# Performance work log

Hardware: AMD Instinct MI355X
Metric: run time of the kernel (lower is better)

The kernel has to match this reference:

```python
import jax, jax.numpy as jnp
import numpy as np

DIM = 256
HEADS = 8
HD = DIM // HEADS          # 32
WS = 8                     # window size
TOPK = 4
SCALE = HD ** -0.5


def setup_inputs() -> dict:
    key = jax.random.key(0)
    k1, k2, k3 = jax.random.split(key, 3)
    B, H, W = 8, 64, 64
    x = jax.random.normal(k1, (B, DIM, H, W), dtype=jnp.float32)
    # 1x1 conv weights (BN folded -> weight + bias), fan-in scaled to keep logits sane
    w_qkv = jax.random.normal(k2, (3 * DIM, DIM), dtype=jnp.float32) / np.sqrt(DIM)
    b_qkv = jnp.zeros((3 * DIM,), dtype=jnp.float32)
    w_proj = jax.random.normal(k3, (DIM, DIM), dtype=jnp.float32) / np.sqrt(DIM)
    b_proj = jnp.zeros((DIM,), dtype=jnp.float32)
    return {"x": x, "w_qkv": w_qkv, "b_qkv": b_qkv, "w_proj": w_proj, "b_proj": b_proj}


def _window_partition(t, ws):
    # t: [BH, D, H, W] -> [BH, R, ws*ws, D]
    bh, d, h, w = t.shape
    gh, gw = h // ws, w // ws
    t = t.reshape(bh, d, gh, ws, gw, ws)
    t = t.transpose(0, 2, 4, 3, 5, 1)          # [BH, gh, gw, ws, ws, D]
    return t.reshape(bh, gh * gw, ws * ws, d)


def reference(x, w_qkv, b_qkv, w_proj, b_proj):
    B, C, H, W = x.shape
    gh, gw = H // WS, W // WS
    R, T = gh * gw, WS * WS
    BH = B * HEADS

    # qkv 1x1 conv
    qkv = jnp.einsum('bchw,oc->bohw', x, w_qkv) + b_qkv[None, :, None, None]
    q, k, v = jnp.split(qkv, 3, axis=1)                       # each [B, C, H, W]

    def to_bh(t):
        return t.reshape(BH, HD, H, W)

    q_w = _window_partition(to_bh(q), WS)                     # [BH, R, T, HD]
    k_w = _window_partition(to_bh(k), WS)
    v_w = _window_partition(to_bh(v), WS)

    # region-level routing: mean-pooled region tokens
    q_r = q_w.mean(axis=2)                                    # [BH, R, HD]
    k_r = k_w.mean(axis=2)
    attn_r = jnp.einsum('brd,bkd->brk', q_r, k_r) * SCALE     # [BH, R, R]
    topk = min(TOPK, R)
    _, topk_idx = jax.lax.top_k(attn_r, topk)                 # [BH, R, K]

    # gather top-k key/value windows per query region
    bidx = jnp.arange(BH)[:, None, None]
    k_sel = k_w[bidx, topk_idx]                               # [BH, R, K, T, HD]
    v_sel = v_w[bidx, topk_idx]
    k_sel = k_sel.reshape(BH, R, topk * T, HD)
    v_sel = v_sel.reshape(BH, R, topk * T, HD)

    # token-level attention inside routed regions
    attn = jnp.einsum('brtd,brsd->brts', q_w, k_sel) * SCALE  # [BH, R, T, K*T]
    attn = jax.nn.softmax(attn, axis=-1)
    out_w = jnp.einsum('brts,brsd->brtd', attn, v_sel)        # [BH, R, T, HD]

    # window reverse -> [BH, HD, H, W]
    out = out_w.reshape(BH, gh, gw, WS, WS, HD)
    out = out.transpose(0, 5, 1, 3, 2, 4).reshape(BH, HD, H, W)
    out = out.reshape(B, C, H, W)

    out = jnp.einsum('bchw,oc->bohw', out, w_proj) + b_proj[None, :, None, None]
    return out
```

## Files before the change

### kernel.cpp

```cpp
#include <hip/hip_runtime.h>
#include <hip/hip_bf16.h>

#define ATT_SCALE 0.17677669529663687f
#define EXP_C1 0.2550349235534668f
#define EXP_C2 23.083120654223400f

typedef short v8s __attribute__((ext_vector_type(8)));
typedef float v4f __attribute__((ext_vector_type(4)));
typedef float v16f __attribute__((ext_vector_type(16)));
typedef const __attribute__((address_space(1))) unsigned int gu32;
typedef __attribute__((address_space(3))) unsigned int lu32;

__device__ __forceinline__ void g2l16(const void* g, void* l) {
  __builtin_amdgcn_global_load_lds((gu32*)g, (lu32*)l, 16, 0, 0);
}

__device__ __forceinline__ float bflo(unsigned u){ union{unsigned i;float f;}x; x.i=u<<16; return x.f; }
__device__ __forceinline__ float bfhi(unsigned u){ union{unsigned i;float f;}x; x.i=u&0xffff0000u; return x.f; }
__device__ __forceinline__ unsigned short bf16r(float v){
  __hip_bfloat16 h = __float2bfloat16(v);
  return *reinterpret_cast<unsigned short*>(&h);
}
__device__ __forceinline__ unsigned pack_bf2(float a, float b){
  return (unsigned)bf16r(a) | ((unsigned)bf16r(b) << 16);
}
__device__ __forceinline__ unsigned cvtpk(float lo, float hi){
  unsigned r;
  asm("v_cvt_pk_bf16_f32 %0, %1, %2" : "=v"(r) : "v"(lo), "v"(hi));
  return r;
}
__device__ __forceinline__ void pl32swap(unsigned &a, unsigned &b){
  asm volatile("v_permlane32_swap_b32 %0, %1" : "+v"(a), "+v"(b));
}

__global__ __launch_bounds__(256) void prep_w(const float* __restrict__ w_qkv,
                                              const float* __restrict__ w_proj,
                                              unsigned short* __restrict__ Wq,
                                              unsigned short* __restrict__ Wp) {
  const int blk = blockIdx.x, t = threadIdx.x;
  const float* src = (blk < 768) ? (w_qkv + blk*256) : (w_proj + (blk-768)*256);
  unsigned short* dst = (blk < 768) ? (Wq + blk*256) : (Wp + (blk-768)*256);
  int col = (t & ~63) | ((t & 63) ^ ((blk & 7) << 3));
  dst[col] = bf16r(src[t]);
}

__global__ __launch_bounds__(256) void prep_x(const float* __restrict__ x,
                                              unsigned short* __restrict__ Xb) {
  __shared__ __align__(16) char hbuf[8192];
  const int blk = blockIdx.x;
  const int b = blk >> 8, cc = (blk >> 6) & 3, pc = blk & 63;
  const int c0 = cc << 6, p0 = pc << 6;
  const int t = threadIdx.x, wv = t >> 6, lane = t & 63;

  float hi[16];
  const float* xp = x + ((size_t)(b*256 + c0 + wv*16))*4096 + p0 + lane;
  #pragma unroll
  for (int i = 0; i < 16; ++i) hi[i] = xp[(size_t)i*4096];
  #pragma unroll
  for (int gi = 0; gi < 2; ++gi) {
    uint4 uh;
    uh.x = pack_bf2(hi[gi*8+0], hi[gi*8+1]); uh.y = pack_bf2(hi[gi*8+2], hi[gi*8+3]);
    uh.z = pack_bf2(hi[gi*8+4], hi[gi*8+5]); uh.w = pack_bf2(hi[gi*8+6], hi[gi*8+7]);
    int off = lane*128 + ((wv*32 + gi*16) ^ ((lane & 7) << 4));
    *(uint4*)(hbuf + off) = uh;
  }
  __syncthreads();
  const size_t rowbase = ((size_t)(b*4096 + p0)) * 512 + (size_t)c0*2;
  #pragma unroll
  for (int s = 0; s < 2; ++s) {
    int gidx = s*256 + t;
    int row = gidx >> 3, gb = (gidx & 7) << 4;
    uint4 vh = *(const uint4*)(hbuf + row*128 + gb);
    *(uint4*)((char*)Xb + rowbase + (size_t)row*512 + gb) = vh;
  }
}

template<int EPI>
__global__ __launch_bounds__(256) void k_gemm(
    const unsigned short* __restrict__ Wstk,
    const unsigned short* __restrict__ Bmat,
    const float* __restrict__ bias,
    unsigned short* __restrict__ qbuf, unsigned short* __restrict__ kbuf,
    unsigned short* __restrict__ vbuf, float* __restrict__ outp) {
  __shared__ __align__(16) char lds[40960];
  const int tid = threadIdx.x;
  const int wv = tid >> 6, lane = tid & 63;
  const int mt = blockIdx.x, nt = blockIdx.y;

  v4f acc[4][4];
  #pragma unroll
  for (int i = 0; i < 4; ++i)
    #pragma unroll
    for (int j = 0; j < 4; ++j) acc[i][j] = (v4f){0.f,0.f,0.f,0.f};

  const char* wlanebase = (const char*)Wstk + ((size_t)(mt*256) + (lane>>3))*512 + (lane&7)*16;
  const size_t prowlane = (size_t)(nt*64 + (lane>>3))*512 + (lane&7)*16;

  for (int kt = 0; kt < 4; ++kt) {
    const int k0b = kt * 128;
    __syncthreads();
    #pragma unroll
    for (int o = 0; o < 8; ++o) {
      int op = wv*8 + o;
      g2l16(wlanebase + (size_t)(op*8)*512 + k0b, lds + op*1024);
    }
    #pragma unroll
    for (int o = 0; o < 2; ++o) {
      int op = wv*2 + o;
      g2l16((const char*)Bmat + prowlane + (size_t)(op*8)*512 + k0b, lds + 32768 + op*1024);
    }
    __syncthreads();
    #pragma unroll
    for (int kk = 0; kk < 2; ++kk) {
      const int kb = kk*64 + ((lane>>4)<<4);
      v8s a[4], b[4];
      #pragma unroll
      for (int i = 0; i < 4; ++i) {
        int mr = wv*64 + i*16 + (lane & 15);
        a[i] = *(const v8s*)(lds + mr*128 + (kb ^ ((mr & 7) << 4)));
      }
      #pragma unroll
      for (int j = 0; j < 4; ++j) {
        int nr = j*16 + (lane & 15);
        b[j] = *(const v8s*)(lds + 32768 + nr*128 + (kb ^ ((nr & 7) << 4)));
      }
      #pragma unroll
      for (int i = 0; i < 4; ++i)
        #pragma unroll
        for (int j = 0; j < 4; ++j)
          acc[i][j] = __builtin_amdgcn_mfma_f32_16x16x32_bf16(a[i], b[j], acc[i][j], 0, 0, 0);
    }
  }

  if (EPI == 0) {
    if (mt < 2) {
      unsigned short* outbuf = (mt == 0) ? qbuf : kbuf;
      #pragma unroll
      for (int i = 0; i < 4; ++i) {
        int o = mt*256 + wv*64 + i*16 + ((lane >> 4) << 2);
        int head = (o >> 5) & 7, d0 = o & 31;
        float b0 = bias[o], b1 = bias[o+1], b2 = bias[o+2], b3 = bias[o+3];
        #pragma unroll
        for (int j = 0; j < 4; ++j) {
          int p = nt*64 + j*16 + (lane & 15);
          int bb = p >> 12, ploc = p & 4095;
          int h = ploc >> 6, w = ploc & 63;
          int rr = ((h >> 3) << 3) | (w >> 3), tt = ((h & 7) << 3) | (w & 7);
          int bh = bb*8 + head;
          uint2 u;
          u.x = pack_bf2(acc[i][j][0] + b0, acc[i][j][1] + b1);
          u.y = pack_bf2(acc[i][j][2] + b2, acc[i][j][3] + b3);
          *(uint2*)(outbuf + (size_t)(((bh << 6) | rr)*64 + tt)*32 + d0) = u;
        }
      }
    } else {
      #pragma unroll
      for (int i = 0; i < 4; ++i) {
        int o = 512 + wv*64 + i*16 + ((lane >> 4) << 2);
        int vch = o - 512;
        int head = vch >> 5, d0 = vch & 31;
        float bv[4] = {bias[o], bias[o+1], bias[o+2], bias[o+3]};
        #pragma unroll
        for (int j = 0; j < 4; ++j) {
          int p = nt*64 + j*16 + (lane & 15);
          int bb = p >> 12, ploc = p & 4095;
          int h = ploc >> 6, w = ploc & 63;
          int rr = ((h >> 3) << 3) | (w >> 3), tt = ((h & 7) << 3) | (w & 7);
          int bh = bb*8 + head;
          size_t base = ((size_t)((bh << 6) | rr)*32 + d0)*64 + tt;
          #pragma unroll
          for (int c = 0; c < 4; ++c)
            vbuf[base + (size_t)c*64] = bf16r(acc[i][j][c] + bv[c]);
        }
      }
    }
  } else {
    #pragma unroll
    for (int i = 0; i < 4; ++i) {
      int o = wv*64 + i*16 + ((lane >> 4) << 2);
      float b0 = bias[o], b1 = bias[o+1], b2 = bias[o+2], b3 = bias[o+3];
      #pragma unroll
      for (int j = 0; j < 4; ++j) {
        int p = nt*64 + j*16 + (lane & 15);
        int bb = p >> 12, ploc = p & 4095;
        float* dst = outp + ((size_t)(bb*256 + o))*4096 + ploc;
        dst[0]     = acc[i][j][0] + b0;
        dst[4096]  = acc[i][j][1] + b1;
        dst[8192]  = acc[i][j][2] + b2;
        dst[12288] = acc[i][j][3] + b3;
      }
    }
  }
}

__global__ __launch_bounds__(256) void k_xmean(const float* __restrict__ x,
                                               float* __restrict__ xmean) {
  __shared__ float part[64][8];
  const int bc = blockIdx.x;
  const int tid = threadIdx.x;
  const int h = tid >> 2, qq = tid & 3;
  const float* xp = x + (size_t)bc*4096 + h*64 + qq*16;
  float s0 = 0.f, s1 = 0.f;
  #pragma unroll
  for (int j = 0; j < 8; ++j) { s0 += xp[j]; s1 += xp[8+j]; }
  part[h][qq*2]   = s0;
  part[h][qq*2+1] = s1;
  __syncthreads();
  if (tid < 64) {
    int rh = tid >> 3, wc = tid & 7;
    float s = 0.f;
    #pragma unroll
    for (int j = 0; j < 8; ++j) s += part[rh*8+j][wc];
    xmean[bc*64 + tid] = s * (1.0f/64.0f);
  }
}

__global__ __launch_bounds__(256) void k_route(const float* __restrict__ xmean,
                                               const float* __restrict__ w_qkv,
                                               const float* __restrict__ b_qkv,
                                               int* __restrict__ topk) {
  __shared__ float xm[128][64];
  __shared__ float qr[64][33];
  __shared__ float kr[64][33];
  const int bh = blockIdx.x, b = bh >> 3, head = bh & 7;
  const int tid = threadIdx.x;
  const int d = tid & 31, r0 = tid >> 5;
  float qacc[8], kacc[8];
  const float bq = b_qkv[head*32 + d], bk = b_qkv[256 + head*32 + d];
  #pragma unroll
  for (int i = 0; i < 8; ++i) { qacc[i] = bq; kacc[i] = bk; }

  for (int c0 = 0; c0 < 256; c0 += 128) {
    __syncthreads();
    #pragma unroll
    for (int i = 0; i < 32; ++i) {
      int idx = i*256 + tid;
      int row = idx >> 6, col = idx & 63;
      xm[row][col] = xmean[(b*256 + c0 + row)*64 + col];
    }
    __syncthreads();
    const float* wqp = w_qkv + (head*32 + d)*256 + c0;
    const float* wkp = w_qkv + (256 + head*32 + d)*256 + c0;
    for (int c = 0; c < 128; ++c) {
      float wq = wqp[c], wk = wkp[c];
      #pragma unroll
      for (int i = 0; i < 8; ++i) {
        float xv = xm[c][r0 + 8*i];
        qacc[i] += wq * xv;
        kacc[i] += wk * xv;
      }
    }
  }
  #pragma unroll
  for (int i = 0; i < 8; ++i) { qr[r0+8*i][d] = qacc[i]; kr[r0+8*i][d] = kacc[i]; }
  __syncthreads();

  float* ar = &xm[0][0];
  for (int item = tid; item < 4096; item += 256) {
    int i = item >> 6, j = item & 63;
    float s = 0.f;
    #pragma unroll
    for (int dd = 0; dd < 32; ++dd) s += qr[i][dd]*kr[j][dd];
    ar[i*64 + j] = s;
  }
  __syncthreads();
  if (tid < 64) {
    for (int kk = 0; kk < 4; ++kk) {
      float best = -3e38f; int bj = 0;
      for (int j = 0; j < 64; ++j) {
        float v = ar[tid*64 + j];
        if (v > best) { best = v; bj = j; }
      }
      ar[tid*64 + bj] = -3e38f;
      topk[(bh*64 + tid)*4 + kk] = bj;
    }
  }
}

__global__ __launch_bounds__(256) void k_attn(const unsigned short* __restrict__ qw,
                                              const unsigned short* __restrict__ kw,
                                              const unsigned short* __restrict__ vwt,
                                              const int* __restrict__ topk,
                                              unsigned short* __restrict__ owt) {
  const int lane = threadIdx.x & 63;
  const int W = blockIdx.x*4 + (threadIdx.x >> 6);
  const int bh = W >> 6, rr = W & 63;
  const int lo5 = lane & 31, hi = lane >> 5;
  const int b = bh >> 3, head = bh & 7;

  const unsigned short* qb = qw + (size_t)(bh*64 + rr)*2048;
  v8s qf[2][2];
  #pragma unroll
  for (int qt = 0; qt < 2; ++qt)
    #pragma unroll
    for (int ck = 0; ck < 2; ++ck)
      qf[qt][ck] = *(const v8s*)(qb + (qt*32 + lo5)*32 + ck*16 + hi*8);

  int idx4[4];
  #pragma unroll
  for (int w = 0; w < 4; ++w) idx4[w] = topk[(bh*64 + rr)*4 + w];

  v16f O[2];
  #pragma unroll
  for (int qt = 0; qt < 2; ++qt)
    #pragma unroll
    for (int r = 0; r < 16; ++r) O[qt][r] = 0.f;
  float lsum[2] = {0.f, 0.f};

  #pragma unroll
  for (int w = 0; w < 4; ++w) {
    const unsigned short* kb = kw  + (size_t)(bh*64 + idx4[w])*2048;
    const unsigned short* vb = vwt + (size_t)(bh*64 + idx4[w])*2048;
    v8s kf[2][2], vf[4];
    #pragma unroll
    for (int kt = 0; kt < 2; ++kt)
      #pragma unroll
      for (int ck = 0; ck < 2; ++ck)
        kf[kt][ck] = *(const v8s*)(kb + (kt*32 + lo5)*32 + ck*16 + hi*8);
    #pragma unroll
    for (int mk = 0; mk < 4; ++mk)
      vf[mk] = *(const v8s*)(vb + lo5*64 + mk*16 + hi*8);

    v16f S[2][2];
    #pragma unroll
    for (int kt = 0; kt < 2; ++kt)
      #pragma unroll
      for (int qt = 0; qt < 2; ++qt) {
        v16f z;
        #pragma unroll
        for (int r = 0; r < 16; ++r) z[r] = 0.f;
        z = __builtin_amdgcn_mfma_f32_32x32x16_bf16(kf[kt][0], qf[qt][0], z, 0, 0, 0);
        S[kt][qt] = __builtin_amdgcn_mfma_f32_32x32x16_bf16(kf[kt][1], qf[qt][1], z, 0, 0, 0);
      }

    #pragma unroll
    for (int kt = 0; kt < 2; ++kt) {
      #pragma unroll
      for (int qt = 0; qt < 2; ++qt) {
        float p[16];
        #pragma unroll
        for (int r = 0; r < 16; ++r)
          p[r] = __builtin_amdgcn_exp2f(__builtin_fmaf(S[kt][qt][r], EXP_C1, -EXP_C2));
        float s01 = (p[0]+p[1]) + (p[2]+p[3]);
        float s23 = (p[4]+p[5]) + (p[6]+p[7]);
        float s45 = (p[8]+p[9]) + (p[10]+p[11]);
        float s67 = (p[12]+p[13]) + (p[14]+p[15]);
        lsum[qt] += (s01 + s23) + (s45 + s67);

        unsigned wh[8], wl[8];
        #pragma unroll
        for (int i = 0; i < 8; ++i) {
          wh[i] = cvtpk(p[2*i], p[2*i+1]);
          float l0 = p[2*i]   - bflo(wh[i]);
          float l1 = p[2*i+1] - bfhi(wh[i]);
          wl[i] = cvtpk(l0, l1);
        }
        pl32swap(wh[0], wh[2]); pl32swap(wh[1], wh[3]);
        pl32swap(wh[4], wh[6]); pl32swap(wh[5], wh[7]);
        pl32swap(wl[0], wl[2]); pl32swap(wl[1], wl[3]);
        pl32swap(wl[4], wl[6]); pl32swap(wl[5], wl[7]);
        union { unsigned u[4]; v8s v; } fA, fB;
        fA.u[0] = wh[0]; fA.u[1] = wh[1]; fA.u[2] = wh[2]; fA.u[3] = wh[3];
        fB.u[0] = wl[0]; fB.u[1] = wl[1]; fB.u[2] = wl[2]; fB.u[3] = wl[3];
        O[qt] = __builtin_amdgcn_mfma_f32_32x32x16_bf16(fA.v, vf[2*kt], O[qt], 0, 0, 0);
        O[qt] = __builtin_amdgcn_mfma_f32_32x32x16_bf16(fB.v, vf[2*kt], O[qt], 0, 0, 0);
        fA.u[0] = wh[4]; fA.u[1] = wh[5]; fA.u[2] = wh[6]; fA.u[3] = wh[7];
        fB.u[0] = wl[4]; fB.u[1] = wl[5]; fB.u[2] = wl[6]; fB.u[3] = wl[7];
        O[qt] = __builtin_amdgcn_mfma_f32_32x32x16_bf16(fA.v, vf[2*kt+1], O[qt], 0, 0, 0);
        O[qt] = __builtin_amdgcn_mfma_f32_32x32x16_bf16(fB.v, vf[2*kt+1], O[qt], 0, 0, 0);
      }
    }
  }

  float linv[2];
  #pragma unroll
  for (int qt = 0; qt < 2; ++qt) {
    float t = lsum[qt] + __shfl_xor(lsum[qt], 32);
    linv[qt] = 1.0f / t;
  }

  #pragma unroll
  for (int qt = 0; qt < 2; ++qt) {
    #pragma unroll
    for (int r = 0; r < 16; ++r) {
      int q = (r & 3) + 8*(r >> 2) + 4*hi;
      float li = __shfl(linv[qt], q);
      float val = O[qt][r] * li;
      int tok = qt*32 + q;
      int h = ((rr >> 3) << 3) | (tok >> 3);
      int wcol = ((rr & 7) << 3) | (tok & 7);
      int pg = (b << 12) | (h << 6) | wcol;
      int col = ((head >> 1) << 6) | ((((head & 1) << 5) + lo5) ^ ((tok & 7) << 3));
      owt[(size_t)pg*256 + col] = bf16r(val);
    }
  }
}

extern "C" void kernel_launch(void* const* d_in, const int* in_sizes, int n_in,
                              void* d_out, int out_size, void* d_ws, size_t ws_size,
                              hipStream_t stream) {
  (void)in_sizes; (void)n_in; (void)out_size; (void)ws_size;
  const float* x      = (const float*)d_in[0];
  const float* w_qkv  = (const float*)d_in[1];
  const float* b_qkv  = (const float*)d_in[2];
  const float* w_proj = (const float*)d_in[3];
  const float* b_proj = (const float*)d_in[4];
  float* out = (float*)d_out;

  char* ws = (char*)d_ws;
  unsigned short* Xb  = (unsigned short*)ws;
  unsigned short* Wq  = (unsigned short*)(ws + 16777216);
  unsigned short* Wp  = (unsigned short*)(ws + 17170432);
  unsigned short* qw  = (unsigned short*)(ws + 17301504);
  unsigned short* kw  = (unsigned short*)(ws + 34078720);
  unsigned short* vwt = (unsigned short*)(ws + 50855936);
  float* xmean        = (float*)(ws + 67633152);
  int* topk           = (int*)(ws + 68157440);
  unsigned short* owt = Xb;

  prep_w <<<dim3(1024), 256, 0, stream>>>(w_qkv, w_proj, Wq, Wp);
  prep_x <<<dim3(2048), 256, 0, stream>>>(x, Xb);
  k_xmean<<<dim3(2048), 256, 0, stream>>>(x, xmean);
  k_route<<<dim3(64),   256, 0, stream>>>(xmean, w_qkv, b_qkv, topk);
  k_gemm<0><<<dim3(3, 512), 256, 0, stream>>>(Wq, Xb, b_qkv, qw, kw, vwt, nullptr);
  k_attn <<<dim3(1024), 256, 0, stream>>>(qw, kw, vwt, topk, owt);
  k_gemm<1><<<dim3(1, 512), 256, 0, stream>>>(Wp, owt, b_proj, nullptr, nullptr, nullptr, out);
}
```

Before: 124.6 us.

## Fuse weight/x prep with region-mean partials; double-buffer GEMM with smaller M tiles

Merges the weight conversion, x transposition and region-mean computation into one prep kernel. Per-window partial sums are produced from the x values already loaded for the bf16 transpose, and k_route finishes the reduction, so the separate k_xmean pass over x goes away. The GEMM now uses 128-row M tiles with double-buffered LDS prefetch, which doubles the grid size for better CU occupancy and overlaps global loads with MFMA. The cost is a larger partials buffer and more redundant B-tile loads across M tiles.

```diff
diff --git a/kernel.cpp b/kernel.cpp
--- a/kernel.cpp
+++ b/kernel.cpp
@@ -33,29 +33,43 @@
   asm volatile("v_permlane32_swap_b32 %0, %1" : "+v"(a), "+v"(b));
 }
 
-__global__ __launch_bounds__(256) void prep_w(const float* __restrict__ w_qkv,
+__global__ __launch_bounds__(256) void k_prep(const float* __restrict__ x,
+                                              const float* __restrict__ w_qkv,
                                               const float* __restrict__ w_proj,
+                                              unsigned short* __restrict__ Xb,
                                               unsigned short* __restrict__ Wq,
-                                              unsigned short* __restrict__ Wp) {
-  const int blk = blockIdx.x, t = threadIdx.x;
-  const float* src = (blk < 768) ? (w_qkv + blk*256) : (w_proj + (blk-768)*256);
-  unsigned short* dst = (blk < 768) ? (Wq + blk*256) : (Wp + (blk-768)*256);
-  int col = (t & ~63) | ((t & 63) ^ ((blk & 7) << 3));
-  dst[col] = bf16r(src[t]);
-}
-
-__global__ __launch_bounds__(256) void prep_x(const float* __restrict__ x,
-                                              unsigned short* __restrict__ Xb) {
+                                              unsigned short* __restrict__ Wp,
+                                              float* __restrict__ part) {
   __shared__ __align__(16) char hbuf[8192];
+  __shared__ float pbuf[512];
   const int blk = blockIdx.x;
+  const int t = threadIdx.x;
+  if (blk >= 2048) {
+    const int m = blk - 2048;
+    const float* src = (m < 768) ? (w_qkv + m*256) : (w_proj + (size_t)(m - 768)*256);
+    unsigned short* dst = (m < 768) ? (Wq + m*256) : (Wp + (size_t)(m - 768)*256);
+    int col = (t & ~63) | ((t & 63) ^ ((m & 7) << 3));
+    dst[col] = bf16r(src[t]);
+    return;
+  }
   const int b = blk >> 8, cc = (blk >> 6) & 3, pc = blk & 63;
   const int c0 = cc << 6, p0 = pc << 6;
-  const int t = threadIdx.x, wv = t >> 6, lane = t & 63;
+  const int wv = t >> 6, lane = t & 63;
 
   float hi[16];
   const float* xp = x + ((size_t)(b*256 + c0 + wv*16))*4096 + p0 + lane;
   #pragma unroll
   for (int i = 0; i < 16; ++i) hi[i] = xp[(size_t)i*4096];
+
+  #pragma unroll
+  for (int i = 0; i < 16; ++i) {
+    float s = hi[i];
+    s += __shfl_xor(s, 1);
+    s += __shfl_xor(s, 2);
+    s += __shfl_xor(s, 4);
+    if ((lane & 7) == 0) pbuf[(wv*16 + i)*8 + (lane >> 3)] = s;
+  }
+
   #pragma unroll
   for (int gi = 0; gi < 2; ++gi) {
     uint4 uh;
@@ -72,6 +86,76 @@
     int row = gidx >> 3, gb = (gidx & 7) << 4;
     uint4 vh = *(const uint4*)(hbuf + row*128 + gb);
     *(uint4*)((char*)Xb + rowbase + (size_t)row*512 + gb) = vh;
+  }
+  const size_t pbase = ((size_t)(b*64 + pc)*256 + c0)*8;
+  part[pbase + t]       = pbuf[t];
+  part[pbase + 256 + t] = pbuf[t + 256];
+}
+
+__global__ __launch_bounds__(256) void k_route(const float* __restrict__ part,
+                                               const float* __restrict__ w_qkv,
+                                               const float* __restrict__ b_qkv,
+                                               int* __restrict__ topk) {
+  __shared__ float xm[128][64];
+  __shared__ float qr[64][33];
+  __shared__ float kr[64][33];
+  const int bh = blockIdx.x, b = bh >> 3, head = bh & 7;
+  const int tid = threadIdx.x;
+  const int d = tid & 31, r0 = tid >> 5;
+  float qacc[8], kacc[8];
+  const float bq = b_qkv[head*32 + d], bk = b_qkv[256 + head*32 + d];
+  #pragma unroll
+  for (int i = 0; i < 8; ++i) { qacc[i] = bq; kacc[i] = bk; }
+
+  for (int c0 = 0; c0 < 256; c0 += 128) {
+    __syncthreads();
+    #pragma unroll
+    for (int i = 0; i < 32; ++i) {
+      int idx = i*256 + tid;
+      int row = idx >> 6, col = idx & 63;
+      int rh = col >> 3, wc = col & 7;
+      const float* pp = part + ((size_t)(b*64 + rh*8)*256 + c0 + row)*8 + wc;
+      float s = 0.f;
+      #pragma unroll
+      for (int j = 0; j < 8; ++j) s += pp[(size_t)j*2048];
+      xm[row][col] = s * 0.015625f;
+    }
+    __syncthreads();
+    const float* wqp = w_qkv + (head*32 + d)*256 + c0;
+    const float* wkp = w_qkv + (256 + head*32 + d)*256 + c0;
+    for (int c = 0; c < 128; ++c) {
+      float wq = wqp[c], wk = wkp[c];
+      #pragma unroll
+      for (int i = 0; i < 8; ++i) {
+        float xv = xm[c][r0 + 8*i];
+        qacc[i] += wq * xv;
+        kacc[i] += wk * xv;
+      }
+    }
+  }
+  #pragma unroll
+  for (int i = 0; i < 8; ++i) { qr[r0+8*i][d] = qacc[i]; kr[r0+8*i][d] = kacc[i]; }
+  __syncthreads();
+
+  float* ar = &xm[0][0];
+  for (int item = tid; item < 4096; item += 256) {
+    int i = item >> 6, j = item & 63;
+    float s = 0.f;
+    #pragma unroll
+    for (int dd = 0; dd < 32; ++dd) s += qr[i][dd]*kr[j][dd];
+    ar[i*64 + j] = s;
+  }
+  __syncthreads();
+  if (tid < 64) {
+    for (int kk = 0; kk < 4; ++kk) {
+      float best = -3e38f; int bj = 0;
+      for (int j = 0; j < 64; ++j) {
+        float v = ar[tid*64 + j];
+        if (v > best) { best = v; bj = j; }
+      }
+      ar[tid*64 + bj] = -3e38f;
+      topk[(bh*64 + tid)*4 + kk] = bj;
+    }
   }
 }
 
@@ -82,62 +166,79 @@
     const float* __restrict__ bias,
     unsigned short* __restrict__ qbuf, unsigned short* __restrict__ kbuf,
     unsigned short* __restrict__ vbuf, float* __restrict__ outp) {
-  __shared__ __align__(16) char lds[40960];
+  __shared__ __align__(16) char lds[49152];
   const int tid = threadIdx.x;
   const int wv = tid >> 6, lane = tid & 63;
   const int mt = blockIdx.x, nt = blockIdx.y;
 
-  v4f acc[4][4];
-  #pragma unroll
-  for (int i = 0; i < 4; ++i)
+  v4f acc[2][4];
+  #pragma unroll
+  for (int i = 0; i < 2; ++i)
     #pragma unroll
     for (int j = 0; j < 4; ++j) acc[i][j] = (v4f){0.f,0.f,0.f,0.f};
 
-  const char* wlanebase = (const char*)Wstk + ((size_t)(mt*256) + (lane>>3))*512 + (lane&7)*16;
-  const size_t prowlane = (size_t)(nt*64 + (lane>>3))*512 + (lane&7)*16;
-
+  const char* wlanebase = (const char*)Wstk + ((size_t)(mt*128) + (lane>>3))*512 + (lane&7)*16;
+  const char* xlanebase = (const char*)Bmat + ((size_t)(nt*64 + (lane>>3))*512 + (lane&7)*16);
+
+  {
+    char* wb = lds; char* xb = lds + 32768;
+    #pragma unroll
+    for (int o = 0; o < 4; ++o) { int op = wv*4 + o; g2l16(wlanebase + (size_t)(op*8)*512, wb + op*1024); }
+    #pragma unroll
+    for (int o = 0; o < 2; ++o) { int op = wv*2 + o; g2l16(xlanebase + (size_t)(op*8)*512, xb + op*1024); }
+  }
+  asm volatile("s_waitcnt vmcnt(0)" ::: "memory");
+  __syncthreads();
+
+  int cur = 0;
+  #pragma unroll
   for (int kt = 0; kt < 4; ++kt) {
-    const int k0b = kt * 128;
-    __syncthreads();
-    #pragma unroll
-    for (int o = 0; o < 8; ++o) {
-      int op = wv*8 + o;
-      g2l16(wlanebase + (size_t)(op*8)*512 + k0b, lds + op*1024);
-    }
-    #pragma unroll
-    for (int o = 0; o < 2; ++o) {
-      int op = wv*2 + o;
-      g2l16((const char*)Bmat + prowlane + (size_t)(op*8)*512 + k0b, lds + 32768 + op*1024);
-    }
-    __syncthreads();
-    #pragma unroll
-    for (int kk = 0; kk < 2; ++kk) {
-      const int kb = kk*64 + ((lane>>4)<<4);
-      v8s a[4], b[4];
-      #pragma unroll
-      for (int i = 0; i < 4; ++i) {
-        int mr = wv*64 + i*16 + (lane & 15);
-        a[i] = *(const v8s*)(lds + mr*128 + (kb ^ ((mr & 7) << 4)));
-      }
-      #pragma unroll
-      for (int j = 0; j < 4; ++j) {
-        int nr = j*16 + (lane & 15);
-        b[j] = *(const v8s*)(lds + 32768 + nr*128 + (kb ^ ((nr & 7) << 4)));
-      }
-      #pragma unroll
-      for (int i = 0; i < 4; ++i)
-        #pragma unroll
-        for (int j = 0; j < 4; ++j)
-          acc[i][j] = __builtin_amdgcn_mfma_f32_16x16x32_bf16(a[i], b[j], acc[i][j], 0, 0, 0);
+    if (kt < 3) {
+      const int k0b = (kt + 1)*128;
+      char* wb = lds + (cur^1)*16384;
+      char* xb = lds + 32768 + (cur^1)*8192;
+      #pragma unroll
+      for (int o = 0; o < 4; ++o) { int op = wv*4 + o; g2l16(wlanebase + (size_t)(op*8)*512 + k0b, wb + op*1024); }
+      #pragma unroll
+      for (int o = 0; o < 2; ++o) { int op = wv*2 + o; g2l16(xlanebase + (size_t)(op*8)*512 + k0b, xb + op*1024); }
+    }
+    {
+      const char* wb = lds + cur*16384;
+      const char* xb = lds + 32768 + cur*8192;
+      #pragma unroll
+      for (int kk = 0; kk < 2; ++kk) {
+        const int kb = kk*64 + ((lane>>4)<<4);
+        v8s a[2], b[4];
+        #pragma unroll
+        for (int i = 0; i < 2; ++i) {
+          int mr = wv*32 + i*16 + (lane & 15);
+          a[i] = *(const v8s*)(wb + mr*128 + (kb ^ ((mr & 7) << 4)));
+        }
+        #pragma unroll
+        for (int j = 0; j < 4; ++j) {
+          int nr = j*16 + (lane & 15);
+          b[j] = *(const v8s*)(xb + nr*128 + (kb ^ ((nr & 7) << 4)));
+        }
+        #pragma unroll
+        for (int i = 0; i < 2; ++i)
+          #pragma unroll
+          for (int j = 0; j < 4; ++j)
+            acc[i][j] = __builtin_amdgcn_mfma_f32_16x16x32_bf16(a[i], b[j], acc[i][j], 0, 0, 0);
+      }
+    }
+    if (kt < 3) {
+      asm volatile("s_waitcnt vmcnt(0)" ::: "memory");
+      __syncthreads();
+      cur ^= 1;
     }
   }
 
   if (EPI == 0) {
-    if (mt < 2) {
-      unsigned short* outbuf = (mt == 0) ? qbuf : kbuf;
-      #pragma unroll
-      for (int i = 0; i < 4; ++i) {
-        int o = mt*256 + wv*64 + i*16 + ((lane >> 4) << 2);
+    if (mt < 4) {
+      unsigned short* outbuf = (mt < 2) ? qbuf : kbuf;
+      #pragma unroll
+      for (int i = 0; i < 2; ++i) {
+        int o = mt*128 + wv*32 + i*16 + ((lane >> 4) << 2);
         int head = (o >> 5) & 7, d0 = o & 31;
         float b0 = bias[o], b1 = bias[o+1], b2 = bias[o+2], b3 = bias[o+3];
         #pragma unroll
@@ -155,8 +256,8 @@
       }
     } else {
       #pragma unroll
-      for (int i = 0; i < 4; ++i) {
-        int o = 512 + wv*64 + i*16 + ((lane >> 4) << 2);
+      for (int i = 0; i < 2; ++i) {
+        int o = mt*128 + wv*32 + i*16 + ((lane >> 4) << 2);
         int vch = o - 512;
         int head = vch >> 5, d0 = vch & 31;
         float bv[4] = {bias[o], bias[o+1], bias[o+2], bias[o+3]};
@@ -176,8 +277,8 @@
     }
   } else {
     #pragma unroll
-    for (int i = 0; i < 4; ++i) {
-      int o = wv*64 + i*16 + ((lane >> 4) << 2);
+    for (int i = 0; i < 2; ++i) {
+      int o = mt*128 + wv*32 + i*16 + ((lane >> 4) << 2);
       float b0 = bias[o], b1 = bias[o+1], b2 = bias[o+2], b3 = bias[o+3];
       #pragma unroll
       for (int j = 0; j < 4; ++j) {
@@ -189,90 +290,6 @@
         dst[8192]  = acc[i][j][2] + b2;
         dst[12288] = acc[i][j][3] + b3;
       }
-    }
-  }
-}
-
-__global__ __launch_bounds__(256) void k_xmean(const float* __restrict__ x,
-                                               float* __restrict__ xmean) {
-  __shared__ float part[64][8];
-  const int bc = blockIdx.x;
-  const int tid = threadIdx.x;
-  const int h = tid >> 2, qq = tid & 3;
-  const float* xp = x + (size_t)bc*4096 + h*64 + qq*16;
-  float s0 = 0.f, s1 = 0.f;
-  #pragma unroll
-  for (int j = 0; j < 8; ++j) { s0 += xp[j]; s1 += xp[8+j]; }
-  part[h][qq*2]   = s0;
-  part[h][qq*2+1] = s1;
-  __syncthreads();
-  if (tid < 64) {
-    int rh = tid >> 3, wc = tid & 7;
-    float s = 0.f;
-    #pragma unroll
-    for (int j = 0; j < 8; ++j) s += part[rh*8+j][wc];
-    xmean[bc*64 + tid] = s * (1.0f/64.0f);
-  }
-}
-
-__global__ __launch_bounds__(256) void k_route(const float* __restrict__ xmean,
-                                               const float* __restrict__ w_qkv,
-                                               const float* __restrict__ b_qkv,
-                                               int* __restrict__ topk) {
-  __shared__ float xm[128][64];
-  __shared__ float qr[64][33];
-  __shared__ float kr[64][33];
-  const int bh = blockIdx.x, b = bh >> 3, head = bh & 7;
-  const int tid = threadIdx.x;
-  const int d = tid & 31, r0 = tid >> 5;
-  float qacc[8], kacc[8];
-  const float bq = b_qkv[head*32 + d], bk = b_qkv[256 + head*32 + d];
-  #pragma unroll
-  for (int i = 0; i < 8; ++i) { qacc[i] = bq; kacc[i] = bk; }
-
-  for (int c0 = 0; c0 < 256; c0 += 128) {
-    __syncthreads();
-    #pragma unroll
-    for (int i = 0; i < 32; ++i) {
-      int idx = i*256 + tid;
-      int row = idx >> 6, col = idx & 63;
-      xm[row][col] = xmean[(b*256 + c0 + row)*64 + col];
-    }
-    __syncthreads();
-    const float* wqp = w_qkv + (head*32 + d)*256 + c0;
-    const float* wkp = w_qkv + (256 + head*32 + d)*256 + c0;
-    for (int c = 0; c < 128; ++c) {
-      float wq = wqp[c], wk = wkp[c];
-      #pragma unroll
-      for (int i = 0; i < 8; ++i) {
-        float xv = xm[c][r0 + 8*i];
-        qacc[i] += wq * xv;
-        kacc[i] += wk * xv;
-      }
-    }
-  }
-  #pragma unroll
-  for (int i = 0; i < 8; ++i) { qr[r0+8*i][d] = qacc[i]; kr[r0+8*i][d] = kacc[i]; }
-  __syncthreads();
-
-  float* ar = &xm[0][0];
-  for (int item = tid; item < 4096; item += 256) {
-    int i = item >> 6, j = item & 63;
-    float s = 0.f;
-    #pragma unroll
-    for (int dd = 0; dd < 32; ++dd) s += qr[i][dd]*kr[j][dd];
-    ar[i*64 + j] = s;
-  }
-  __syncthreads();
-  if (tid < 64) {
-    for (int kk = 0; kk < 4; ++kk) {
-      float best = -3e38f; int bj = 0;
-      for (int j = 0; j < 64; ++j) {
-        float v = ar[tid*64 + j];
-        if (v > best) { best = v; bj = j; }
-      }
-      ar[tid*64 + bj] = -3e38f;
-      topk[(bh*64 + tid)*4 + kk] = bj;
     }
   }
 }
@@ -414,15 +431,13 @@
   unsigned short* qw  = (unsigned short*)(ws + 17301504);
   unsigned short* kw  = (unsigned short*)(ws + 34078720);
   unsigned short* vwt = (unsigned short*)(ws + 50855936);
-  float* xmean        = (float*)(ws + 67633152);
-  int* topk           = (int*)(ws + 68157440);
+  float* part         = (float*)(ws + 67633152);
+  int* topk           = (int*)(ws + 71827456);
   unsigned short* owt = Xb;
 
-  prep_w <<<dim3(1024), 256, 0, stream>>>(w_qkv, w_proj, Wq, Wp);
-  prep_x <<<dim3(2048), 256, 0, stream>>>(x, Xb);
-  k_xmean<<<dim3(2048), 256, 0, stream>>>(x, xmean);
-  k_route<<<dim3(64),   256, 0, stream>>>(xmean, w_qkv, b_qkv, topk);
-  k_gemm<0><<<dim3(3, 512), 256, 0, stream>>>(Wq, Xb, b_qkv, qw, kw, vwt, nullptr);
+  k_prep <<<dim3(3072), 256, 0, stream>>>(x, w_qkv, w_proj, Xb, Wq, Wp, part);
+  k_route<<<dim3(64),   256, 0, stream>>>(part, w_qkv, b_qkv, topk);
+  k_gemm<0><<<dim3(6, 512), 256, 0, stream>>>(Wq, Xb, b_qkv, qw, kw, vwt, nullptr);
   k_attn <<<dim3(1024), 256, 0, stream>>>(qw, kw, vwt, topk, owt);
-  k_gemm<1><<<dim3(1, 512), 256, 0, stream>>>(Wp, owt, b_proj, nullptr, nullptr, nullptr, out);
-}
+  k_gemm<1><<<dim3(2, 512), 256, 0, stream>>>(Wp, owt, b_proj, nullptr, nullptr, nullptr, out);
+}
```

Measured after the change: 131.0 us. +5.1%, slower.
